# Performance work log

Measured on AMD Instinct MI355X. Metric: run time of the kernel, lower is better.

Reference implementation:

```python
import jax, jax.numpy as jnp
import numpy as np

B, T, D = 2, 2048, 2048
H, HD = 16, 128          # n_heads, head_dim (D = H * HD)
THETA = 10000.0
TOPK_RATIO = 0.55
EPS = 1e-5


def _ste(x, q):
    # straight-through estimator: forward = q, backward = identity
    return x + jax.lax.stop_gradient(q - x)


def ternary_weight(w):
    # absmean ternary quantization to {-1, 0, +1} * scale
    scale = jnp.mean(jnp.abs(w))
    wq = jnp.clip(jnp.round(w / (scale + EPS)), -1.0, 1.0) * scale
    return _ste(w, wq)


def quant_int(x, bits):
    # per-token (last-dim) absmax quantization to signed `bits`-bit grid
    qmax = 2.0 ** (bits - 1) - 1.0
    s = qmax / jnp.clip(jnp.max(jnp.abs(x), axis=-1, keepdims=True), EPS, None)
    q = jnp.clip(jnp.round(x * s), -qmax - 1.0, qmax) / s
    return _ste(x, q)


def topk_sparsify(x, ratio):
    # keep top-k values by magnitude per token, zero the rest
    d = x.shape[-1]
    k = max(1, int(ratio * d))
    flat = x.reshape(-1, d)
    _, idx = jax.lax.top_k(jnp.abs(flat), k)
    mask = jnp.zeros_like(flat).at[jnp.arange(flat.shape[0])[:, None], idx].set(1.0)
    return (flat * _ste(jnp.ones_like(flat), mask)).reshape(x.shape)


def bitlinear(x, w, act_mode):
    if act_mode == 'int4':
        x = quant_int(x, 4)
    elif act_mode == 'topk_int8':
        x = quant_int(topk_sparsify(x, TOPK_RATIO), 8)
    return x @ ternary_weight(w).T


def rope(x):
    # x: (B, H, T, hd); rotate-half RoPE with cat([freqs, freqs]) layout
    hd, t = x.shape[-1], x.shape[2]
    inv = 1.0 / THETA ** (jnp.arange(0, hd, 2, dtype=jnp.float32) / hd)
    freqs = jnp.arange(t, dtype=jnp.float32)[:, None] * inv[None, :]  # (T, hd/2)
    emb = jnp.concatenate([freqs, freqs], axis=-1)                     # (T, hd)
    cos = jnp.cos(emb)[None, None]
    sin = jnp.sin(emb)[None, None]
    x1, x2 = x[..., : hd // 2], x[..., hd // 2 :]
    rot = jnp.concatenate([-x2, x1], axis=-1)
    return x * cos + rot * sin


def setup_inputs() -> dict:
    key = jax.random.key(0)
    ks = jax.random.split(key, 5)
    return {
        'x': jax.random.normal(ks[0], (B, T, D), dtype=jnp.float32),
        'wq': jax.random.normal(ks[1], (D, D), dtype=jnp.float32) * 0.02,
        'wk': jax.random.normal(ks[2], (D, D), dtype=jnp.float32) * 0.02,
        'wv': jax.random.normal(ks[3], (D, D), dtype=jnp.float32) * 0.02,
        'wo': jax.random.normal(ks[4], (D, D), dtype=jnp.float32) * 0.02,
    }


def reference(x, wq, wk, wv, wo):
    b, t, _ = x.shape
    q = bitlinear(x, wq, 'int4').reshape(b, t, H, HD).transpose(0, 2, 1, 3)
    k = bitlinear(x, wk, 'int4').reshape(b, t, H, HD).transpose(0, 2, 1, 3)
    v = bitlinear(x, wv, 'int4').reshape(b, t, H, HD).transpose(0, 2, 1, 3)
    q = rope(q)
    k = rope(k)
    # bidirectional SDPA, no mask
    scores = jnp.einsum('bhqd,bhkd->bhqk', q, k) / jnp.sqrt(jnp.float32(HD))
    attn = jax.nn.softmax(scores, axis=-1)
    out = jnp.einsum('bhqk,bhkd->bhqd', attn, v)
    out = out.transpose(0, 2, 1, 3).reshape(b, t, H * HD)
    return bitlinear(out, wo, 'topk_int8')
```

## Files before the change

### kernel.cpp

```cpp
#include <hip/hip_runtime.h>
#include <stdint.h>
#include <math.h>


typedef __attribute__((ext_vector_type(8))) short short8;
typedef __attribute__((ext_vector_type(4))) int i32x4;
typedef __attribute__((ext_vector_type(8))) _Float16 f16x8;
typedef __attribute__((ext_vector_type(16))) float f32x16;

#define GLDS16(g, l)                                                        \
  __builtin_amdgcn_global_load_lds(                                         \
      (const __attribute__((address_space(1))) void*)(g),                   \
      (__attribute__((address_space(3))) void*)(l), 16, 0, 0)

__device__ __forceinline__ unsigned short f2bf(float v) {
  return (unsigned short)(__float_as_uint(v) >> 16);
}

__global__ __launch_bounds__(256) void k_costab(float* __restrict__ ct,
                                                float* __restrict__ st) {
  int idx = blockIdx.x * 256 + threadIdx.x;
  int t = idx >> 6, i = idx & 63;
  float f = (float)(2 * i) / 128.0f;
  float inv = 1.0f / powf(10000.0f, f);
  float fr = (float)t * inv;
  ct[idx] = cosf(fr);
  st[idx] = sinf(fr);
}

__global__ __launch_bounds__(256) void k_wsum(const float* __restrict__ w0,
                                              const float* __restrict__ w1,
                                              const float* __restrict__ w2,
                                              const float* __restrict__ w3,
                                              double* __restrict__ part) {
  int bx = blockIdx.x;
  int mat = bx >> 10;
  const float* w = (mat == 0) ? w0 : (mat == 1) ? w1 : (mat == 2) ? w2 : w3;
  int base = (bx & 1023) * 4096;
  double s = 0.0;
#pragma unroll
  for (int i = 0; i < 16; ++i)
    s += (double)fabsf(w[base + threadIdx.x + i * 256]);
  __shared__ double red[256];
  red[threadIdx.x] = s;
  __syncthreads();
  for (int off = 128; off; off >>= 1) {
    if (threadIdx.x < off) red[threadIdx.x] += red[threadIdx.x + off];
    __syncthreads();
  }
  if (threadIdx.x == 0) part[bx] = red[0];
}

__global__ __launch_bounds__(256) void k_wscale(const double* __restrict__ part,
                                                float* __restrict__ wsc) {
  int m = blockIdx.x, tid = threadIdx.x;
  const double* p = part + m * 1024;
  double s = p[tid] + p[tid + 256] + p[tid + 512] + p[tid + 768];
  __shared__ double red[256];
  red[tid] = s;
  __syncthreads();
  for (int off = 128; off; off >>= 1) {
    if (tid < off) red[tid] += red[tid + off];
    __syncthreads();
  }
  if (tid == 0) wsc[m] = (float)(red[0] / 4194304.0);
}

__global__ __launch_bounds__(256) void k_wquant(const float* __restrict__ w0,
                                                const float* __restrict__ w1,
                                                const float* __restrict__ w2,
                                                const float* __restrict__ w3,
                                                const float* __restrict__ wsc,
                                                signed char* __restrict__ wt) {
  int mat = blockIdx.y;
  const float* w = (mat == 0) ? w0 : (mat == 1) ? w1 : (mat == 2) ? w2 : w3;
  float se = wsc[mat] + 1e-5f;
  size_t base = (size_t)blockIdx.x * 4096;
  signed char* o = wt + (size_t)mat * 4194304 + base;
  const float* wp = w + base;
#pragma unroll 4
  for (int i = 0; i < 16; ++i) {
    int idx = threadIdx.x + i * 256;
    float v = rintf(wp[idx] / se);
    v = fminf(fmaxf(v, -1.0f), 1.0f);
    o[idx] = (signed char)v;
  }
}

__global__ __launch_bounds__(256) void k_xquant(const float* __restrict__ x,
                                                signed char* __restrict__ xq,
                                                float* __restrict__ sx) {
  int row = blockIdx.x, tid = threadIdx.x;
  const float* xr = x + (size_t)row * 2048;
  float v[8];
  float mx = 0.0f;
#pragma unroll
  for (int i = 0; i < 8; ++i) {
    v[i] = xr[tid + i * 256];
    mx = fmaxf(mx, fabsf(v[i]));
  }
  __shared__ float red[256];
  red[tid] = mx;
  __syncthreads();
  for (int off = 128; off; off >>= 1) {
    if (tid < off) red[tid] = fmaxf(red[tid], red[tid + off]);
    __syncthreads();
  }
  float s = 7.0f / fmaxf(red[0], 1e-5f);
#pragma unroll
  for (int i = 0; i < 8; ++i) {
    float q = rintf(v[i] * s);
    q = fminf(fmaxf(q, -8.0f), 7.0f);
    xq[(size_t)row * 2048 + tid + i * 256] = (signed char)q;
  }
  if (tid == 0) sx[row] = s;
}

__global__ __launch_bounds__(256) void k_gemm3(const signed char* __restrict__ A,
                                               const signed char* __restrict__ wtall,
                                               float* __restrict__ qo,
                                               float* __restrict__ vo,
                                               _Float16* __restrict__ khp,
                                               _Float16* __restrict__ klp,
                                               const float* __restrict__ srow,
                                               const float* __restrict__ wsc,
                                               const float* __restrict__ ct,
                                               const float* __restrict__ st) {
  __shared__ alignas(16) signed char As[128 * 64];
  __shared__ alignas(16) signed char Bs[128 * 64];
  __shared__ float fac[128];
  const int tid = threadIdx.x, wave = tid >> 6, lane = tid & 63;
  const int bxi = blockIdx.x;
  const int mat = bxi >> 4;
  const signed char* Bw = wtall + (size_t)mat * 4194304;
  const int brow = blockIdx.y * 128, bcol = (bxi & 15) * 128;
  if (tid < 128) fac[tid] = wsc[mat] / srow[brow + tid];
  const int wr = wave >> 1, wc = wave & 1;
  i32x4 acc[4][4];
#pragma unroll
  for (int m = 0; m < 4; ++m)
#pragma unroll
    for (int n = 0; n < 4; ++n) acc[m][n] = (i32x4){0, 0, 0, 0};
  const int srl = tid >> 2;
  const int ssw = ((tid & 3) ^ ((srl >> 1) & 3)) * 16;
  const signed char* Ag = A + (size_t)(brow + srl) * 2048 + ssw;
  const signed char* Bg = Bw + (size_t)(bcol + srl) * 2048 + ssw;
  char* AsB = (char*)As + wave * 1024;
  char* BsB = (char*)Bs + wave * 1024;
  const int fr = lane & 15, kb = lane >> 4;
  const int rsl = (kb ^ ((fr >> 1) & 3)) * 16;
  for (int k0 = 0; k0 < 2048; k0 += 64) {
    __syncthreads();
    GLDS16(Ag + k0, AsB);
    GLDS16(Ag + k0 + (size_t)64 * 2048, AsB + 4096);
    GLDS16(Bg + k0, BsB);
    GLDS16(Bg + k0 + (size_t)64 * 2048, BsB + 4096);
    __syncthreads();
    i32x4 af[4], bf[4];
#pragma unroll
    for (int m = 0; m < 4; ++m)
      af[m] = *(const i32x4*)&As[(wr * 64 + m * 16 + fr) * 64 + rsl];
#pragma unroll
    for (int n = 0; n < 4; ++n)
      bf[n] = *(const i32x4*)
           &Bs[(wc * 32 + (n & 1) * 16 + (n >> 1) * 64 + fr) * 64 + rsl];
#pragma unroll
    for (int m = 0; m < 4; ++m)
#pragma unroll
      for (int n = 0; n < 4; ++n)
        acc[m][n] = __builtin_amdgcn_mfma_i32_16x16x64_i8(af[m], bf[n],
                                                          acc[m][n], 0, 0, 0);
  }
  const int fq = lane >> 4;
  if (mat == 2) {
#pragma unroll
    for (int m = 0; m < 4; ++m)
#pragma unroll
      for (int n = 0; n < 4; ++n) {
        int col = bcol + wc * 32 + (n & 1) * 16 + (n >> 1) * 64 + fr;
#pragma unroll
        for (int r = 0; r < 4; ++r) {
          int row = wr * 64 + m * 16 + fq * 4 + r;
          vo[(size_t)(brow + row) * 2048 + col] = (float)acc[m][n][r] * fac[row];
        }
      }
  } else {
    const int hh = bcol >> 7;
#pragma unroll
    for (int m = 0; m < 4; ++m)
#pragma unroll
      for (int n = 0; n < 2; ++n) {
        int d1 = wc * 32 + n * 16 + fr;
#pragma unroll
        for (int r = 0; r < 4; ++r) {
          int row = wr * 64 + m * 16 + fq * 4 + r;
          int rg = brow + row;
          int t = rg & 2047, bb = rg >> 11;
          float c = ct[t * 64 + d1], sn = st[t * 64 + d1];
          float x1 = (float)acc[m][n][r] * fac[row];
          float x2 = (float)acc[m][n + 2][r] * fac[row];
          float y1 = x1 * c - x2 * sn;
          float y2 = x2 * c + x1 * sn;
          if (mat == 0) {
            qo[(size_t)rg * 2048 + bcol + d1] = y1;
            qo[(size_t)rg * 2048 + bcol + d1 + 64] = y2;
          } else {
            size_t ob = ((size_t)(bb * 16 + hh) * 2048 + t) * 128 + d1;
            _Float16 h1 = (_Float16)y1, h2 = (_Float16)y2;
            khp[ob] = h1;
            khp[ob + 64] = h2;
            klp[ob] = (_Float16)(y1 - (float)h1);
            klp[ob + 64] = (_Float16)(y2 - (float)h2);
          }
        }
      }
  }
}

__global__ __launch_bounds__(256) void k_gemm(const signed char* __restrict__ A,
                                              const signed char* __restrict__ Bw,
                                              float* __restrict__ C,
                                              const float* __restrict__ srow,
                                              const float* __restrict__ wsp) {
  __shared__ alignas(16) signed char As[128 * 64];
  __shared__ alignas(16) signed char Bs[128 * 64];
  __shared__ float fac[128];
  const int tid = threadIdx.x, wave = tid >> 6, lane = tid & 63;
  const int brow = blockIdx.y * 128, bcol = blockIdx.x * 128;
  if (tid < 128) fac[tid] = wsp[0] / srow[brow + tid];
  const int wr = wave >> 1, wc = wave & 1;
  i32x4 acc[4][4];
#pragma unroll
  for (int m = 0; m < 4; ++m)
#pragma unroll
    for (int n = 0; n < 4; ++n) acc[m][n] = (i32x4){0, 0, 0, 0};
  const int srl = tid >> 2;
  const int ssw = ((tid & 3) ^ ((srl >> 1) & 3)) * 16;
  const signed char* Ag = A + (size_t)(brow + srl) * 2048 + ssw;
  const signed char* Bg = Bw + (size_t)(bcol + srl) * 2048 + ssw;
  char* AsB = (char*)As + wave * 1024;
  char* BsB = (char*)Bs + wave * 1024;
  const int fr = lane & 15, kb = lane >> 4;
  const int rsl = (kb ^ ((fr >> 1) & 3)) * 16;
  for (int k0 = 0; k0 < 2048; k0 += 64) {
    __syncthreads();
    GLDS16(Ag + k0, AsB);
    GLDS16(Ag + k0 + (size_t)64 * 2048, AsB + 4096);
    GLDS16(Bg + k0, BsB);
    GLDS16(Bg + k0 + (size_t)64 * 2048, BsB + 4096);
    __syncthreads();
    i32x4 af[4], bf[4];
#pragma unroll
    for (int m = 0; m < 4; ++m)
      af[m] = *(const i32x4*)&As[(wr * 64 + m * 16 + fr) * 64 + rsl];
#pragma unroll
    for (int n = 0; n < 4; ++n)
      bf[n] = *(const i32x4*)&Bs[(wc * 64 + n * 16 + fr) * 64 + rsl];
#pragma unroll
    for (int m = 0; m < 4; ++m)
#pragma unroll
      for (int n = 0; n < 4; ++n)
        acc[m][n] = __builtin_amdgcn_mfma_i32_16x16x64_i8(af[m], bf[n],
                                                          acc[m][n], 0, 0, 0);
  }
  const int fq = lane >> 4;
#pragma unroll
  for (int m = 0; m < 4; ++m)
#pragma unroll
    for (int n = 0; n < 4; ++n)
#pragma unroll
      for (int r = 0; r < 4; ++r) {
        int row = wr * 64 + m * 16 + fq * 4 + r;
        C[(size_t)(brow + row) * 2048 + bcol + wc * 64 + n * 16 + fr] =
            (float)acc[m][n][r] * fac[row];
      }
}

__global__ __launch_bounds__(256) void k_vtrans(const float* __restrict__ vb,
                                                _Float16* __restrict__ vth,
                                                _Float16* __restrict__ vtl) {
  __shared__ float F[64][133];
  const int tid = threadIdx.x;
  const int bh = blockIdx.y, b = bh >> 4, h = bh & 15;
  const int t0 = blockIdx.x * 64;
  {
    const int tr = tid >> 2, tc = (tid & 3) * 32;
    const float* src = vb + ((size_t)(b * 2048 + t0 + tr)) * 2048 + h * 128 + tc;
#pragma unroll
    for (int j = 0; j < 8; ++j) {
      float4 v = *(const float4*)(src + j * 4);
      F[tr][tc + j * 4 + 0] = v.x;
      F[tr][tc + j * 4 + 1] = v.y;
      F[tr][tc + j * 4 + 2] = v.z;
      F[tr][tc + j * 4 + 3] = v.w;
    }
  }
  __syncthreads();
  {
    const int vd = tid >> 1, th = (tid & 1) * 32;
    f16x8 oh[4], ol[4];
#pragma unroll
    for (int j = 0; j < 32; ++j) {
      float x = F[th + j][vd];
      _Float16 hv = (_Float16)x;
      oh[j >> 3][j & 7] = hv;
      ol[j >> 3][j & 7] = (_Float16)(x - (float)hv);
    }
    _Float16* dh = vth + ((size_t)bh * 128 + vd) * 2048 + t0 + th;
    _Float16* dl = vtl + ((size_t)bh * 128 + vd) * 2048 + t0 + th;
#pragma unroll
    for (int j4 = 0; j4 < 4; ++j4) {
      *(f16x8*)(dh + j4 * 8) = oh[j4];
      *(f16x8*)(dl + j4 * 8) = ol[j4];
    }
  }
}

__global__ __launch_bounds__(256, 2) void k_attn(float* __restrict__ qb,
                                                 const _Float16* __restrict__ kh,
                                                 const _Float16* __restrict__ kl,
                                                 const _Float16* __restrict__ vth,
                                                 const _Float16* __restrict__ vtl) {
  __shared__ alignas(16) char KS[2][2][32 * 256];
  __shared__ alignas(16) char VS[2][2][128 * 88];
  const int tid = threadIdx.x;
  const int wave = tid >> 6, lane = tid & 63;
  const int rl = lane & 31, hi = lane >> 5, hi8 = hi * 8;
  const int bid = blockIdx.x;
  const int xcd = bid & 7, li = bid >> 3;
  const int bh = xcd * 4 + (li >> 4), qt = li & 15;
  const int b = bh >> 4, h = bh & 15;
  const size_t rowbase = (size_t)b * 2048;
  const int hcol = h * 128;
  const float F = 0.08838834764831845f * 1.44269504088896f;
  const float THR = 11.5415603f;

  f16x8 qh[8], ql[8];
  {
    const float* qsrc =
        qb + (rowbase + qt * 128 + wave * 32 + rl) * 2048 + hcol + hi8;
#pragma unroll
    for (int ds = 0; ds < 8; ++ds) {
      float4 a = *(const float4*)(qsrc + ds * 16);
      float4 c = *(const float4*)(qsrc + ds * 16 + 4);
      float v[8] = {a.x, a.y, a.z, a.w, c.x, c.y, c.z, c.w};
      f16x8 hh, ll;
#pragma unroll
      for (int i = 0; i < 8; ++i) {
        float sv = v[i] * F;
        _Float16 hv = (_Float16)sv;
        hh[i] = hv;
        ll[i] = (_Float16)(sv - (float)hv);
      }
      qh[ds] = hh;
      ql[ds] = ll;
    }
  }

  const int kr = tid >> 3, kseg = tid & 7;
  const int vd = tid >> 1, vh2 = tid & 1;
  const _Float16* kbh = kh + ((size_t)bh * 2048 + kr) * 128 + kseg * 16;
  const _Float16* kbl = kl + ((size_t)bh * 2048 + kr) * 128 + kseg * 16;
  const _Float16* vbh = vth + ((size_t)bh * 128 + vd) * 2048 + vh2 * 16;
  const _Float16* vbl = vtl + ((size_t)bh * 128 + vd) * 2048 + vh2 * 16;
  const int kwa0 = kr * 256 + (((2 * kseg) ^ (kr & 7)) << 4);
  const int kwa1 = kr * 256 + (((2 * kseg + 1) ^ (kr & 7)) << 4);
  const int vwa0 = vd * 88 + 2 * vh2 * 16;
  const int vwa1 = vwa0 + 16;

  f16x8 pkh0 = *(const f16x8*)(kbh), pkh1 = *(const f16x8*)(kbh + 8);
  f16x8 pkl0 = *(const f16x8*)(kbl), pkl1 = *(const f16x8*)(kbl + 8);
  f16x8 pvh0 = *(const f16x8*)(vbh), pvh1 = *(const f16x8*)(vbh + 8);
  f16x8 pvl0 = *(const f16x8*)(vbl), pvl1 = *(const f16x8*)(vbl + 8);

  f32x16 Oa[4];
#pragma unroll
  for (int df = 0; df < 4; ++df)
#pragma unroll
    for (int i = 0; i < 16; ++i) Oa[df][i] = 0.0f;
  float m = -INFINITY, lsum = 0.0f;

  for (int kt = 0; kt < 64; ++kt) {
    const int bf = kt & 1;
    *(f16x8*)(KS[bf][0] + kwa0) = pkh0;
    *(f16x8*)(KS[bf][0] + kwa1) = pkh1;
    *(f16x8*)(KS[bf][1] + kwa0) = pkl0;
    *(f16x8*)(KS[bf][1] + kwa1) = pkl1;
    *(f16x8*)(VS[bf][0] + vwa0) = pvh0;
    *(f16x8*)(VS[bf][0] + vwa1) = pvh1;
    *(f16x8*)(VS[bf][1] + vwa0) = pvl0;
    *(f16x8*)(VS[bf][1] + vwa1) = pvl1;
    __syncthreads();
    f32x16 sA = {}, sB = {}, sC = {};
#pragma unroll
    for (int ds = 0; ds < 8; ++ds) {
      const int ra = rl * 256 + (((2 * ds + hi) ^ (rl & 7)) << 4);
      f16x8 ah = *(const f16x8*)(KS[bf][0] + ra);
      f16x8 al = *(const f16x8*)(KS[bf][1] + ra);
      sA = __builtin_amdgcn_mfma_f32_32x32x16_f16(ah, qh[ds], sA, 0, 0, 0);
      sB = __builtin_amdgcn_mfma_f32_32x32x16_f16(ah, ql[ds], sB, 0, 0, 0);
      sC = __builtin_amdgcn_mfma_f32_32x32x16_f16(al, qh[ds], sC, 0, 0, 0);
    }
    if (kt < 63) {
      const _Float16* nkh = kbh + (size_t)(kt + 1) * 4096;
      const _Float16* nkl = kbl + (size_t)(kt + 1) * 4096;
      const _Float16* nvh = vbh + (size_t)(kt + 1) * 32;
      const _Float16* nvl = vbl + (size_t)(kt + 1) * 32;
      pkh0 = *(const f16x8*)(nkh);
      pkh1 = *(const f16x8*)(nkh + 8);
      pkl0 = *(const f16x8*)(nkl);
      pkl1 = *(const f16x8*)(nkl + 8);
      pvh0 = *(const f16x8*)(nvh);
      pvh1 = *(const f16x8*)(nvh + 8);
      pvl0 = *(const f16x8*)(nvl);
      pvl1 = *(const f16x8*)(nvl + 8);
    }
    f32x16 s;
#pragma unroll
    for (int i = 0; i < 16; ++i) s[i] = (sA[i] + sB[i]) + sC[i];
    float pm = fmaxf(
        fmaxf(fmaxf(fmaxf(s[0], s[1]), fmaxf(s[2], s[3])),
              fmaxf(fmaxf(s[4], s[5]), fmaxf(s[6], s[7]))),
        fmaxf(fmaxf(fmaxf(s[8], s[9]), fmaxf(s[10], s[11])),
              fmaxf(fmaxf(s[12], s[13]), fmaxf(s[14], s[15]))));
    pm = fmaxf(pm, __shfl_xor(pm, 32));
    float alpha = 1.0f;
    if (__any(pm > m + THR)) {
      float mn = fmaxf(m, pm);
      alpha = exp2f(m - mn);
      m = mn;
#pragma unroll
      for (int reg = 0; reg < 16; ++reg) {
        int qr = (reg & 3) + 8 * (reg >> 2) + 4 * hi;
        float av = __shfl(alpha, qr);
        Oa[0][reg] *= av;
        Oa[1][reg] *= av;
        Oa[2][reg] *= av;
        Oa[3][reg] *= av;
      }
    }
    unsigned int pkhh[4][2], pkll[4][2];
    float ls = 0.0f;
#pragma unroll
    for (int t4 = 0; t4 < 4; ++t4)
#pragma unroll
      for (int c2 = 0; c2 < 2; ++c2) {
        float pa = exp2f(s[4 * t4 + 2 * c2] - m);
        float pb = exp2f(s[4 * t4 + 2 * c2 + 1] - m);
        ls += pa + pb;
        auto hp = __builtin_amdgcn_cvt_pkrtz(pa, pb);
        float la = pa - (float)hp[0], lb = pb - (float)hp[1];
        auto lp = __builtin_amdgcn_cvt_pkrtz(la, lb);
        pkhh[t4][c2] = __builtin_bit_cast(unsigned int, hp);
        pkll[t4][c2] = __builtin_bit_cast(unsigned int, lp);
      }
    ls += __shfl_xor(ls, 32);
    lsum = lsum * alpha + ls;
    f16x8 paH[2], paL[2];
#pragma unroll
    for (int hf = 0; hf < 2; ++hf) {
      {
        unsigned int a0 = pkhh[2 * hf][0], b0 = pkhh[2 * hf + 1][0];
        unsigned int a1 = pkhh[2 * hf][1], b1 = pkhh[2 * hf + 1][1];
        asm("v_permlane32_swap_b32 %0, %1" : "+v"(a0), "+v"(b0));
        asm("v_permlane32_swap_b32 %0, %1" : "+v"(a1), "+v"(b1));
        uint4 u;
        u.x = a0; u.y = a1; u.z = b0; u.w = b1;
        paH[hf] = __builtin_bit_cast(f16x8, u);
      }
      {
        unsigned int a0 = pkll[2 * hf][0], b0 = pkll[2 * hf + 1][0];
        unsigned int a1 = pkll[2 * hf][1], b1 = pkll[2 * hf + 1][1];
        asm("v_permlane32_swap_b32 %0, %1" : "+v"(a0), "+v"(b0));
        asm("v_permlane32_swap_b32 %0, %1" : "+v"(a1), "+v"(b1));
        uint4 u;
        u.x = a0; u.y = a1; u.z = b0; u.w = b1;
        paL[hf] = __builtin_bit_cast(f16x8, u);
      }
    }
#pragma unroll
    for (int df = 0; df < 4; ++df) {
#pragma unroll
      for (int hf = 0; hf < 2; ++hf) {
        const int va = (df * 32 + rl) * 88 + ((2 * hf + hi) << 4);
        f16x8 vh = *(const f16x8*)(VS[bf][0] + va);
        f16x8 vl = *(const f16x8*)(VS[bf][1] + va);
        Oa[df] = __builtin_amdgcn_mfma_f32_32x32x16_f16(paH[hf], vh, Oa[df], 0, 0, 0);
        Oa[df] = __builtin_amdgcn_mfma_f32_32x32x16_f16(paH[hf], vl, Oa[df], 0, 0, 0);
        Oa[df] = __builtin_amdgcn_mfma_f32_32x32x16_f16(paL[hf], vh, Oa[df], 0, 0, 0);
      }
    }
  }
  float linv = 1.0f / lsum;
  float* obase = qb + (rowbase + qt * 128 + wave * 32) * 2048 + hcol;
#pragma unroll
  for (int reg = 0; reg < 16; ++reg) {
    int qr = (reg & 3) + 8 * (reg >> 2) + 4 * hi;
    float lv = __shfl(linv, qr);
    float* orow = obase + (size_t)qr * 2048;
    orow[0 * 32 + rl] = Oa[0][reg] * lv;
    orow[1 * 32 + rl] = Oa[1][reg] * lv;
    orow[2 * 32 + rl] = Oa[2][reg] * lv;
    orow[3 * 32 + rl] = Oa[3][reg] * lv;
  }
}

__global__ __launch_bounds__(256) void k_topk(const float* __restrict__ ain,
                                              signed char* __restrict__ oq,
                                              float* __restrict__ so) {
  const int row = blockIdx.x, tid = threadIdx.x;
  const float* xr = ain + (size_t)row * 2048;
  __shared__ unsigned int bits[2048];
  __shared__ unsigned int hist[256];
  __shared__ unsigned int scn[256];
  __shared__ unsigned int stat[3];
#pragma unroll
  for (int j = 0; j < 8; ++j) {
    int i = tid * 8 + j;
    bits[i] = __float_as_uint(xr[i]) & 0x7fffffffu;
  }
  unsigned int mx = 0;
#pragma unroll
  for (int j = 0; j < 8; ++j) mx = max(mx, bits[tid * 8 + j]);
  scn[tid] = mx;
  __syncthreads();
  for (int off = 128; off; off >>= 1) {
    if (tid < off) scn[tid] = max(scn[tid], scn[tid + off]);
    __syncthreads();
  }
  if (tid == 0) { stat[0] = 0u; stat[1] = 1126u; stat[2] = scn[0]; }
  for (int p = 0; p < 4; ++p) {
    const int shift = 24 - 8 * p;
    hist[tid] = 0u;
    __syncthreads();
    unsigned int pref = stat[0];
    unsigned int rk0 = stat[1];
#pragma unroll
    for (int j = 0; j < 8; ++j) {
      unsigned int u = bits[tid * 8 + j];
      bool match = (p == 0) || ((u >> (shift + 8)) == pref);
      if (match) atomicAdd(&hist[(u >> shift) & 255u], 1u);
    }
    __syncthreads();
    scn[tid] = hist[tid];
    __syncthreads();
    for (int off = 1; off < 256; off <<= 1) {
      unsigned int v = (tid + off < 256) ? scn[tid + off] : 0u;
      __syncthreads();
      scn[tid] += v;
      __syncthreads();
    }
    unsigned int nxt = (tid == 255) ? 0u : scn[tid + 1];
    if (scn[tid] >= rk0 && nxt < rk0) {
      stat[0] = (pref << 8) | (unsigned int)tid;
      stat[1] = rk0 - nxt;
    }
    __syncthreads();
  }
  const unsigned int T = stat[0];
  const unsigned int rkeep = stat[1];
  const float rowmax = __uint_as_float(stat[2]);
  const float s = 127.0f / fmaxf(rowmax, 1e-5f);
  unsigned int cnt = 0;
#pragma unroll
  for (int j = 0; j < 8; ++j) cnt += (bits[tid * 8 + j] == T) ? 1u : 0u;
  scn[tid] = cnt;
  __syncthreads();
  for (int off = 1; off < 256; off <<= 1) {
    unsigned int v = (tid >= off) ? scn[tid - off] : 0u;
    __syncthreads();
    scn[tid] += v;
    __syncthreads();
  }
  unsigned int eqr = scn[tid] - cnt;
#pragma unroll
  for (int j = 0; j < 8; ++j) {
    int i = tid * 8 + j;
    unsigned int u = bits[i];
    bool keep = u > T;
    if (u == T) { keep = (eqr < rkeep); eqr++; }
    float q = 0.0f;
    if (keep) {
      q = rintf(xr[i] * s);
      q = fminf(fmaxf(q, -128.0f), 127.0f);
    }
    oq[(size_t)row * 2048 + i] = (signed char)q;
  }
  if (tid == 0) so[row] = s;
}

extern "C" void kernel_launch(void* const* d_in, const int* in_sizes, int n_in,
                              void* d_out, int out_size, void* d_ws,
                              size_t ws_size, hipStream_t stream) {
  const float* x = (const float*)d_in[0];
  const float* wq = (const float*)d_in[1];
  const float* wk = (const float*)d_in[2];
  const float* wv = (const float*)d_in[3];
  const float* wo = (const float*)d_in[4];
  float* out = (float*)d_out;

  char* ws = (char*)d_ws;
  size_t off = 0;
  auto alloc = [&](size_t bytes) -> void* {
    void* p = ws + off;
    off += (bytes + 255) & ~(size_t)255;
    return p;
  };
  signed char* wt = (signed char*)alloc(4ull * 2048 * 2048);
  signed char* xq = (signed char*)alloc(4096ull * 2048);
  float* qb = (float*)alloc(4096ull * 2048 * 4);
  float* vb = (float*)alloc(4096ull * 2048 * 4);
  _Float16* kh = (_Float16*)alloc(32ull * 2048 * 128 * 2);
  _Float16* kl = (_Float16*)alloc(32ull * 2048 * 128 * 2);
  _Float16* vth = (_Float16*)alloc(32ull * 128 * 2048 * 2);
  _Float16* vtl = (_Float16*)alloc(32ull * 128 * 2048 * 2);
  float* ct = (float*)alloc(2048ull * 64 * 4);
  float* st = (float*)alloc(2048ull * 64 * 4);
  float* sx = (float*)alloc(4096 * 4);
  float* so = (float*)alloc(4096 * 4);
  float* wsc = (float*)alloc(4 * 4);
  double* prt = (double*)alloc(4096 * 8);
  signed char* oq = (signed char*)vb;

  k_costab<<<512, 256, 0, stream>>>(ct, st);
  k_wsum<<<4096, 256, 0, stream>>>(wq, wk, wv, wo, prt);
  k_wscale<<<4, 256, 0, stream>>>(prt, wsc);
  k_wquant<<<dim3(1024, 4), 256, 0, stream>>>(wq, wk, wv, wo, wsc, wt);
  k_xquant<<<4096, 256, 0, stream>>>(x, xq, sx);

  k_gemm3<<<dim3(48, 32), 256, 0, stream>>>(xq, wt, qb, vb, kh, kl, sx, wsc,
                                            ct, st);
  k_vtrans<<<dim3(32, 32), 256, 0, stream>>>(vb, vth, vtl);
  k_attn<<<512, 256, 0, stream>>>(qb, kh, kl, vth, vtl);
  k_topk<<<4096, 256, 0, stream>>>(qb, oq, so);
  k_gemm<<<dim3(16, 32), 256, 0, stream>>>(oq, wt + 3ull * 4194304, out, so,
                                           wsc + 3);
}
```

Baseline: 444.7 us.

## Stream K/V tiles into LDS with direct global-to-LDS loads in attention

The attention kernel used to stage the next K/V tile through registers and then write it to LDS with vector stores. It now issues global_load_lds DMA loads straight into the other LDS buffer right after the barrier, which removes the register staging and the explicit LDS store instructions. The XOR swizzle moves to the global-side addressing, and the V tile drops its 88-byte padded row stride for a 64-byte swizzled layout to avoid bank conflicts. s_setprio is raised around the MFMA blocks to favour matrix issue. The change relies on the barrier's implicit wait covering the asynchronous LDS writes.

```diff
diff --git a/kernel.cpp b/kernel.cpp
--- a/kernel.cpp
+++ b/kernel.cpp
@@ -322,7 +322,7 @@
                                                  const _Float16* __restrict__ vth,
                                                  const _Float16* __restrict__ vtl) {
   __shared__ alignas(16) char KS[2][2][32 * 256];
-  __shared__ alignas(16) char VS[2][2][128 * 88];
+  __shared__ alignas(16) char VS[2][2][128 * 64];
   const int tid = threadIdx.x;
   const int wave = tid >> 6, lane = tid & 63;
   const int rl = lane & 31, hi = lane >> 5, hi8 = hi * 8;
@@ -357,21 +357,20 @@
     }
   }
 
-  const int kr = tid >> 3, kseg = tid & 7;
-  const int vd = tid >> 1, vh2 = tid & 1;
-  const _Float16* kbh = kh + ((size_t)bh * 2048 + kr) * 128 + kseg * 16;
-  const _Float16* kbl = kl + ((size_t)bh * 2048 + kr) * 128 + kseg * 16;
-  const _Float16* vbh = vth + ((size_t)bh * 128 + vd) * 2048 + vh2 * 16;
-  const _Float16* vbl = vtl + ((size_t)bh * 128 + vd) * 2048 + vh2 * 16;
-  const int kwa0 = kr * 256 + (((2 * kseg) ^ (kr & 7)) << 4);
-  const int kwa1 = kr * 256 + (((2 * kseg + 1) ^ (kr & 7)) << 4);
-  const int vwa0 = vd * 88 + 2 * vh2 * 16;
-  const int vwa1 = vwa0 + 16;
-
-  f16x8 pkh0 = *(const f16x8*)(kbh), pkh1 = *(const f16x8*)(kbh + 8);
-  f16x8 pkl0 = *(const f16x8*)(kbl), pkl1 = *(const f16x8*)(kbl + 8);
-  f16x8 pvh0 = *(const f16x8*)(vbh), pvh1 = *(const f16x8*)(vbh + 8);
-  f16x8 pvl0 = *(const f16x8*)(vbl), pvl1 = *(const f16x8*)(vbl + 8);
+  const int krl = lane >> 4, ksl = lane & 15;
+  const int vrl = lane >> 2, vsl = lane & 3;
+  size_t kofs[2], vofs[2];
+#pragma unroll
+  for (int i = 0; i < 2; ++i) {
+    int krow = wave * 8 + i * 4 + krl;
+    kofs[i] = (size_t)krow * 128 + ((ksl ^ (krow & 7)) << 3);
+    int vrow = wave * 32 + i * 16 + vrl;
+    vofs[i] = (size_t)vrow * 2048 + ((vsl ^ (vrow & 3)) << 3);
+  }
+  const _Float16* gkh = kh + (size_t)bh * 262144;
+  const _Float16* gkl = kl + (size_t)bh * 262144;
+  const _Float16* gvh = vth + (size_t)bh * 262144;
+  const _Float16* gvl = vtl + (size_t)bh * 262144;
 
   f32x16 Oa[4];
 #pragma unroll
@@ -380,18 +379,38 @@
     for (int i = 0; i < 16; ++i) Oa[df][i] = 0.0f;
   float m = -INFINITY, lsum = 0.0f;
 
+  {
+#pragma unroll
+    for (int i = 0; i < 2; ++i) {
+      GLDS16(gkh + kofs[i], KS[0][0] + wave * 2048 + i * 1024);
+      GLDS16(gkl + kofs[i], KS[0][1] + wave * 2048 + i * 1024);
+      GLDS16(gvh + vofs[i], VS[0][0] + wave * 2048 + i * 1024);
+      GLDS16(gvl + vofs[i], VS[0][1] + wave * 2048 + i * 1024);
+    }
+  }
+
   for (int kt = 0; kt < 64; ++kt) {
     const int bf = kt & 1;
-    *(f16x8*)(KS[bf][0] + kwa0) = pkh0;
-    *(f16x8*)(KS[bf][0] + kwa1) = pkh1;
-    *(f16x8*)(KS[bf][1] + kwa0) = pkl0;
-    *(f16x8*)(KS[bf][1] + kwa1) = pkl1;
-    *(f16x8*)(VS[bf][0] + vwa0) = pvh0;
-    *(f16x8*)(VS[bf][0] + vwa1) = pvh1;
-    *(f16x8*)(VS[bf][1] + vwa0) = pvl0;
-    *(f16x8*)(VS[bf][1] + vwa1) = pvl1;
-    __syncthreads();
+    __syncthreads();
+    if (kt < 63) {
+      const _Float16* pkh = gkh + (size_t)(kt + 1) * 4096;
+      const _Float16* pkl = gkl + (size_t)(kt + 1) * 4096;
+      const _Float16* pvh = gvh + (size_t)(kt + 1) * 32;
+      const _Float16* pvl = gvl + (size_t)(kt + 1) * 32;
+      char* kd0 = KS[bf ^ 1][0] + wave * 2048;
+      char* kd1 = KS[bf ^ 1][1] + wave * 2048;
+      char* vd0 = VS[bf ^ 1][0] + wave * 2048;
+      char* vd1 = VS[bf ^ 1][1] + wave * 2048;
+#pragma unroll
+      for (int i = 0; i < 2; ++i) {
+        GLDS16(pkh + kofs[i], kd0 + i * 1024);
+        GLDS16(pkl + kofs[i], kd1 + i * 1024);
+        GLDS16(pvh + vofs[i], vd0 + i * 1024);
+        GLDS16(pvl + vofs[i], vd1 + i * 1024);
+      }
+    }
     f32x16 sA = {}, sB = {}, sC = {};
+    __builtin_amdgcn_s_setprio(1);
 #pragma unroll
     for (int ds = 0; ds < 8; ++ds) {
       const int ra = rl * 256 + (((2 * ds + hi) ^ (rl & 7)) << 4);
@@ -401,20 +420,7 @@
       sB = __builtin_amdgcn_mfma_f32_32x32x16_f16(ah, ql[ds], sB, 0, 0, 0);
       sC = __builtin_amdgcn_mfma_f32_32x32x16_f16(al, qh[ds], sC, 0, 0, 0);
     }
-    if (kt < 63) {
-      const _Float16* nkh = kbh + (size_t)(kt + 1) * 4096;
-      const _Float16* nkl = kbl + (size_t)(kt + 1) * 4096;
-      const _Float16* nvh = vbh + (size_t)(kt + 1) * 32;
-      const _Float16* nvl = vbl + (size_t)(kt + 1) * 32;
-      pkh0 = *(const f16x8*)(nkh);
-      pkh1 = *(const f16x8*)(nkh + 8);
-      pkl0 = *(const f16x8*)(nkl);
-      pkl1 = *(const f16x8*)(nkl + 8);
-      pvh0 = *(const f16x8*)(nvh);
-      pvh1 = *(const f16x8*)(nvh + 8);
-      pvl0 = *(const f16x8*)(nvl);
-      pvl1 = *(const f16x8*)(nvl + 8);
-    }
+    __builtin_amdgcn_s_setprio(0);
     f32x16 s;
 #pragma unroll
     for (int i = 0; i < 16; ++i) s[i] = (sA[i] + sB[i]) + sC[i];
@@ -478,11 +484,12 @@
         paL[hf] = __builtin_bit_cast(f16x8, u);
       }
     }
+    __builtin_amdgcn_s_setprio(1);
 #pragma unroll
     for (int df = 0; df < 4; ++df) {
 #pragma unroll
       for (int hf = 0; hf < 2; ++hf) {
-        const int va = (df * 32 + rl) * 88 + ((2 * hf + hi) << 4);
+        const int va = (df * 32 + rl) * 64 + (((2 * hf + hi) ^ (rl & 3)) << 4);
         f16x8 vh = *(const f16x8*)(VS[bf][0] + va);
         f16x8 vl = *(const f16x8*)(VS[bf][1] + va);
         Oa[df] = __builtin_amdgcn_mfma_f32_32x32x16_f16(paH[hf], vh, Oa[df], 0, 0, 0);
@@ -490,6 +497,7 @@
         Oa[df] = __builtin_amdgcn_mfma_f32_32x32x16_f16(paL[hf], vh, Oa[df], 0, 0, 0);
       }
     }
+    __builtin_amdgcn_s_setprio(0);
   }
   float linv = 1.0f / lsum;
   float* obase = qb + (rowbase + qt * 128 + wave * 32) * 2048 + hcol;
```

After: 442.3 us. No clear change (-0.6%).
